# Kernel tuning notes

Hardware: AMD Instinct MI355X
Metric: run time of the kernel (lower is better)

## Reference

```python
import jax, jax.numpy as jnp
import numpy as np

B, T, I = 256, 512, 12   # batch, n_step, input_dims
H, Z = 1024, 128         # hidden_dims, z1_dims


def _gru_step(h, xt, Wih, Whh, bih, bhh):
    # torch GRU/GRUCell gate math; gate order in weights: r, z, n
    gi = xt @ Wih.T + bih            # [B, 3H]
    gh = h @ Whh.T + bhh             # [B, 3H]
    i_r, i_z, i_n = jnp.split(gi, 3, axis=-1)
    h_r, h_z, h_n = jnp.split(gh, 3, axis=-1)
    r = jax.nn.sigmoid(i_r + h_r)
    zg = jax.nn.sigmoid(i_z + h_z)
    n = jnp.tanh(i_n + r * h_n)
    return (1.0 - zg) * n + zg * h


def setup_inputs() -> dict:
    key = jax.random.key(0)
    ks = jax.random.split(key, 24)
    s = 0.03
    d = {
        "x": jax.random.uniform(ks[0], (B, T, I), dtype=jnp.float32),
        "noise": jax.random.normal(ks[1], (B, Z), dtype=jnp.float32),
        # bidirectional GRU encoder (forward / backward directions)
        "W_ih_f": jax.random.normal(ks[2], (3 * H, I)) * s,
        "W_hh_f": jax.random.normal(ks[3], (3 * H, H)) * s,
        "b_ih_f": jnp.zeros((3 * H,), jnp.float32),
        "b_hh_f": jnp.zeros((3 * H,), jnp.float32),
        "W_ih_b": jax.random.normal(ks[4], (3 * H, I)) * s,
        "W_hh_b": jax.random.normal(ks[5], (3 * H, H)) * s,
        "b_ih_b": jnp.zeros((3 * H,), jnp.float32),
        "b_hh_b": jnp.zeros((3 * H,), jnp.float32),
        # mu / var heads over concatenated bidirectional final state [B, 2H]
        "W_mu": jax.random.normal(ks[6], (Z, 2 * H)) * s,
        "b_mu": jnp.zeros((Z,), jnp.float32),
        "W_var": jax.random.normal(ks[7], (Z, 2 * H)) * s,
        "b_var": jnp.zeros((Z,), jnp.float32),
        # decoder
        "W_init": jax.random.normal(ks[8], (H, Z)) * s,
        "b_init": jnp.zeros((H,), jnp.float32),
        "W_out": jax.random.normal(ks[9], (I, H)) * s,
        "b_out": jnp.zeros((I,), jnp.float32),
        "Wc_ih": jax.random.normal(ks[10], (3 * H, I + Z)) * s,
        "Wc_hh": jax.random.normal(ks[11], (3 * H, H)) * s,
        "bc_ih": jnp.zeros((3 * H,), jnp.float32),
        "bc_hh": jnp.zeros((3 * H,), jnp.float32),
    }
    return d


def reference(x, noise, W_ih_f, W_hh_f, b_ih_f, b_hh_f,
              W_ih_b, W_hh_b, b_ih_b, b_hh_b,
              W_mu, b_mu, W_var, b_var,
              W_init, b_init, W_out, b_out,
              Wc_ih, Wc_hh, bc_ih, bc_hh):
    b, t, i = x.shape
    h0 = jnp.zeros((b, W_hh_f.shape[1]), x.dtype)
    xs = jnp.swapaxes(x, 0, 1)  # [T, B, I]

    # ---- encoder: bidirectional GRU, keep only final hidden per direction ----
    def step_f(h, xt):
        return _gru_step(h, xt, W_ih_f, W_hh_f, b_ih_f, b_hh_f), None

    def step_b(h, xt):
        return _gru_step(h, xt, W_ih_b, W_hh_b, b_ih_b, b_hh_b), None

    h_f, _ = jax.lax.scan(step_f, h0, xs)
    h_b, _ = jax.lax.scan(step_b, h0, xs[::-1])
    henc = jnp.concatenate([h_f, h_b], axis=-1)  # [B, 2H] (dir-major, matches torch view)

    mean = henc @ W_mu.T + b_mu
    stddev = jnp.exp(0.5 * (henc @ W_var.T + b_var))
    z = mean + stddev * noise  # rsample (training mode)

    # ---- decoder: GRUCell with teacher forcing (eps starts at 1 -> p < eps) ----
    init_out = jnp.zeros((b, i), x.dtype).at[:, -1].set(1.0)
    teacher = jnp.concatenate([init_out[:, None, :], x[:, :-1, :]], axis=1)  # [B,T,I]
    inps = jnp.swapaxes(teacher, 0, 1)  # [T, B, I]

    hx = jnp.tanh(z @ W_init.T + b_init)

    def dstep(h, inp):
        u = jnp.concatenate([inp, z], axis=1)  # [B, I+Z]
        h = _gru_step(h, u, Wc_ih, Wc_hh, bc_ih, bc_hh)
        out = jax.nn.sigmoid(h @ W_out.T + b_out)
        return h, out

    _, outs = jax.lax.scan(dstep, hx, inps)  # outs: [T, B, I]
    recon = jnp.swapaxes(outs, 0, 1)  # [B, T, I]
    return recon, mean, stddev
```

## Files before the change

kernel.cpp:

```cpp
#include <hip/hip_runtime.h>
#include <cstdint>
#include <cstddef>


typedef _Float16 f16;
typedef _Float16 f16x8 __attribute__((ext_vector_type(8)));
typedef float f32x4 __attribute__((ext_vector_type(4)));

#define NB 256
#define NT 512
#define NI 12
#define NH 1024
#define NZ 128
#define NG 3072
#define KE_ENC 1056
#define KE_DEC 1184
#define XK_ENC 32
#define XK_DEC 160
#define ZXP 40

#define MFMA16(a, b, c) __builtin_amdgcn_mfma_f32_16x16x32_f16((a), (b), (c), 0, 0, 0)

#define OFF_WMF   ((size_t)0)
#define OFF_WMB   (OFF_WMF + (size_t)NG * KE_ENC * 2)
#define OFF_WMD   (OFF_WMB + (size_t)NG * KE_ENC * 2)
#define OFF_WNF   (OFF_WMD + (size_t)NG * KE_DEC * 2)
#define OFF_WNB   (OFF_WNF + (size_t)NH * XK_ENC * 2)
#define OFF_WND   (OFF_WNB + (size_t)NH * XK_ENC * 2)
#define OFF_WOUT  (OFF_WND + (size_t)NH * XK_DEC * 2)
#define OFF_HENC16 (OFF_WOUT + (size_t)16 * KE_ENC * 2)
#define OFF_HF32   (OFF_HENC16 + (size_t)4 * NB * NH * 2)
#define OFF_CTL    (OFF_HF32 + (size_t)2 * NB * NH * 4)
#define OFF_H32D   (OFF_CTL + (size_t)2 * NB * NH * 2)
#define OFF_Z32    (OFF_H32D + (size_t)NB * NH * 4)
#define OFF_Z16    (OFF_Z32 + (size_t)NB * NZ * 4)
#define OFF_FLG    (OFF_Z16 + (size_t)NB * NZ * 2)
#define N_FLG 204800
#define N_FLGD 131072
#define WS_NEEDED (OFF_FLG + (size_t)N_FLG * 4)

#define OUT_MEAN (NB * NT * NI)
#define OUT_STD  (OUT_MEAN + NB * NZ)

__device__ __forceinline__ void wave_spin(const unsigned* base, unsigned tgt,
                                          int lane, int nslots) {
    const unsigned* p = base + (lane & (nslots - 1));
    for (;;) {
        unsigned v = __hip_atomic_load(p, __ATOMIC_RELAXED, __HIP_MEMORY_SCOPE_AGENT);
        if (__all((int)(v == tgt))) break;
        __builtin_amdgcn_s_sleep(1);
    }
}

#define PW(N) do { \
    asm volatile("s_waitcnt vmcnt(%0)" :: "n"(N) : "memory"); \
    __builtin_amdgcn_sched_barrier(0x387); \
} while (0)

__global__ __launch_bounds__(256) void prep_kernel(
    const float* __restrict__ Whhf, const float* __restrict__ Wihf,
    const float* __restrict__ bihf, const float* __restrict__ bhhf,
    const float* __restrict__ Whhb, const float* __restrict__ Wihb,
    const float* __restrict__ bihb, const float* __restrict__ bhhb,
    const float* __restrict__ Wchh, const float* __restrict__ Wcih,
    const float* __restrict__ bcih, const float* __restrict__ bchh,
    const float* __restrict__ Wo,   const float* __restrict__ bo,
    f16* __restrict__ wmf, f16* __restrict__ wmb, f16* __restrict__ wmd,
    f16* __restrict__ wnf, f16* __restrict__ wnb, f16* __restrict__ wnd,
    f16* __restrict__ wout,
    f16* __restrict__ h16e0f, f16* __restrict__ h16e0b,
    unsigned* __restrict__ flgs, unsigned* __restrict__ flgd)
{
    const int gsz = gridDim.x * blockDim.x;
    const int gid = blockIdx.x * blockDim.x + threadIdx.x;

    for (int idx = gid; idx < NG * KE_ENC; idx += gsz) {
        const int c = idx / KE_ENC, k = idx - c * KE_ENC;
        float vf, vb;
        if (k < NH) { vf = Whhf[c * NH + k]; vb = Whhb[c * NH + k]; }
        else {
            const int e = k - NH;
            if (c < 2 * NH) {
                if (e < 12)       { vf = Wihf[c * 12 + e]; vb = Wihb[c * 12 + e]; }
                else if (e == 12) { vf = bihf[c] + bhhf[c]; vb = bihb[c] + bhhb[c]; }
                else              { vf = 0.f; vb = 0.f; }
            } else {
                vf = (e == 12) ? bhhf[c] : 0.f;
                vb = (e == 12) ? bhhb[c] : 0.f;
            }
        }
        wmf[idx] = (f16)vf; wmb[idx] = (f16)vb;
    }
    for (int idx = gid; idx < NG * KE_DEC; idx += gsz) {
        const int c = idx / KE_DEC, k = idx - c * KE_DEC;
        float v;
        if (k < NH) v = Wchh[c * NH + k];
        else {
            const int e = k - NH;
            if (c < 2 * NH) {
                if (e < 12)       v = Wcih[c * 140 + e];
                else if (e == 12) v = bcih[c] + bchh[c];
                else if (e < 32)  v = 0.f;
                else              v = Wcih[c * 140 + 12 + (e - 32)];
            } else v = (e == 12) ? bchh[c] : 0.f;
        }
        wmd[idx] = (f16)v;
    }
    for (int idx = gid; idx < NH * XK_ENC; idx += gsz) {
        const int j = idx >> 5, e = idx & 31;
        const int c = 2 * NH + j;
        float vf, vb;
        if (e < 12)       { vf = Wihf[c * 12 + e]; vb = Wihb[c * 12 + e]; }
        else if (e == 12) { vf = bihf[c]; vb = bihb[c]; }
        else              { vf = 0.f; vb = 0.f; }
        wnf[idx] = (f16)vf; wnb[idx] = (f16)vb;
    }
    for (int idx = gid; idx < NH * XK_DEC; idx += gsz) {
        const int j = idx / XK_DEC, e = idx - j * XK_DEC;
        const int c = 2 * NH + j;
        float v;
        if (e < 12)       v = Wcih[c * 140 + e];
        else if (e == 12) v = bcih[c];
        else if (e < 32)  v = 0.f;
        else              v = Wcih[c * 140 + 12 + (e - 32)];
        wnd[idx] = (f16)v;
    }
    for (int idx = gid; idx < 16 * KE_ENC; idx += gsz) {
        const int i = idx / KE_ENC, k = idx - i * KE_ENC;
        float v = 0.f;
        if (i < 12) {
            if (k < NH) v = Wo[i * NH + k];
            else if (k == NH + 12) v = bo[i];
        }
        wout[idx] = (f16)v;
    }
    for (int idx = gid; idx < NB * NH; idx += gsz) {
        h16e0f[idx] = (f16)0.f; h16e0b[idx] = (f16)0.f;
    }
    for (int idx = gid; idx < N_FLG; idx += gsz) flgs[idx] = 0u;
    for (int idx = gid; idx < N_FLGD; idx += gsz) flgd[idx] = 0u;
}

__global__ __launch_bounds__(256, 1) void enc_kernel(
    const float* __restrict__ x,
    const f16* __restrict__ wmF, const f16* __restrict__ wmB_,
    const f16* __restrict__ wnF, const f16* __restrict__ wnB_,
    f16* __restrict__ hbuf,
    float* __restrict__ hf32,
    unsigned* __restrict__ flg)
{
    constexpr int KE  = KE_ENC;
    constexpr int KEP = KE + 8;

    __shared__ f16 Wlds[48 * KEP];
    __shared__ f16 wext[48 * 36];
    __shared__ f16 wnlds[32 * ZXP];
    __shared__ f16 Zx[64 * ZXP];

    const int tid = threadIdx.x;
    const int bid = blockIdx.x;
    const int w = tid >> 6, lane = tid & 63;
    const int lr = lane & 15, quad = lane >> 4;

    const int chain = bid >> 5;
    const int slice = bid & 31;
    const int dir = chain >> 2;
    const int m0 = (chain & 3) * 64;
    const int j0 = slice * 32;
    const int RB = m0 + (w << 4);

    const f16* wm = dir ? wmB_ : wmF;
    const f16* wn = dir ? wnB_ : wnF;
    f16* hb0 = hbuf + (size_t)dir * 2 * NB * NH;

    constexpr int KQ = KE / 8;
    for (int u = tid; u < 48 * KQ; u += 256) {
        const int r = u / KQ, kk = u - r * KQ;
        const int c = (r >> 4) * NH + j0 + (r & 15);
        *(uint4*)&Wlds[r * KEP + kk * 8] = *(const uint4*)(wm + (size_t)c * KE + kk * 8);
    }
    for (int u = tid; u < 48 * 4; u += 256) {
        const int r = u >> 2, kk = u & 3;
        const int c = (r >> 4) * NH + j0 + 16 + (r & 15);
        *(uint4*)&wext[r * 36 + kk * 8] = *(const uint4*)(wm + (size_t)c * KE + 1024 + kk * 8);
    }
    for (int u = tid; u < 32 * 4; u += 256) {
        const int r = u >> 2, kk = u & 3;
        *(uint4*)&wnlds[r * ZXP + kk * 8] = *(const uint4*)(wn + (size_t)(j0 + r) * XK_ENC + kk * 8);
    }
    for (int u = tid; u < 64 * ZXP / 8; u += 256)
        *(uint4*)&Zx[u * 8] = make_uint4(0u, 0u, 0u, 0u);
    __syncthreads();

    float hmast[2][4];
#pragma unroll
    for (int cs = 0; cs < 2; ++cs)
#pragma unroll
        for (int r = 0; r < 4; ++r) hmast[cs][r] = 0.f;

    unsigned* myflg = flg + (size_t)chain * 512 * 32;

    const char* bg0 = (const char*)wm + 2 * ((size_t)(0 * NH + j0 + 16 + lr) * KE + (quad << 3));
    const char* bg1 = (const char*)wm + 2 * ((size_t)(1 * NH + j0 + 16 + lr) * KE + (quad << 3));
    const char* bg2 = (const char*)wm + 2 * ((size_t)(2 * NH + j0 + 16 + lr) * KE + (quad << 3));

#define EA(c) do { \
    asm volatile( \
        "global_load_dwordx4 %0, %2, off offset:%3 sc0 sc1\n\t" \
        "global_load_dwordx4 %1, %2, off offset:%4 sc0 sc1" \
        : "=&v"(av[(c) & 7][0]), "=&v"(av[(c) & 7][1]) \
        : "v"(ga0), "n"((c) * 128), "n"((c) * 128 + 64) \
        : "memory"); \
} while (0)
#define EB(c) do { \
    asm volatile( \
        "global_load_dwordx4 %0, %6, off offset:%9\n\t" \
        "global_load_dwordx4 %1, %6, off offset:%10\n\t" \
        "global_load_dwordx4 %2, %7, off offset:%9\n\t" \
        "global_load_dwordx4 %3, %7, off offset:%10\n\t" \
        "global_load_dwordx4 %4, %8, off offset:%9\n\t" \
        "global_load_dwordx4 %5, %8, off offset:%10" \
        : "=&v"(bv[(c) & 3][0]), "=&v"(bv[(c) & 3][1]), \
          "=&v"(bv[(c) & 3][2]), "=&v"(bv[(c) & 3][3]), \
          "=&v"(bv[(c) & 3][4]), "=&v"(bv[(c) & 3][5]) \
        : "v"(bg0), "v"(bg1), "v"(bg2), "n"((c) * 128), "n"((c) * 128 + 64) \
        : "memory"); \
} while (0)
#define ECONS(c) do { \
    _Pragma("unroll") \
    for (int kt2_ = 0; kt2_ < 2; ++kt2_) { \
        const int ktg_ = (c) * 2 + kt2_; \
        const f16x8 a_ = av[(c) & 7][kt2_]; \
        _Pragma("unroll") \
        for (int g_ = 0; g_ < 3; ++g_) { \
            const f16x8 bl_ = *(const f16x8*)(&Wlds[(g_ * 16 + lr) * KEP + ktg_ * 32 + (quad << 3)]); \
            acc0[g_] = MFMA16(a_, bl_, acc0[g_]); \
            acc1[g_] = MFMA16(a_, bv[(c) & 3][g_ * 2 + kt2_], acc1[g_]); \
        } \
    } \
} while (0)

#pragma unroll 1
    for (int t = 0; t < NT; ++t) {
        if (tid < 64) {
            f16 rowv[16];
            const int b_ = m0 + tid;
            const int tx = dir ? (NT - 1 - t) : t;
            const float4* xr = (const float4*)(x + ((size_t)b_ * NT + tx) * NI);
            const float4 x0 = xr[0], x1 = xr[1], x2 = xr[2];
            rowv[0] = (f16)x0.x; rowv[1] = (f16)x0.y; rowv[2] = (f16)x0.z; rowv[3] = (f16)x0.w;
            rowv[4] = (f16)x1.x; rowv[5] = (f16)x1.y; rowv[6] = (f16)x1.z; rowv[7] = (f16)x1.w;
            rowv[8] = (f16)x2.x; rowv[9] = (f16)x2.y; rowv[10] = (f16)x2.z; rowv[11] = (f16)x2.w;
            rowv[12] = (f16)1.f; rowv[13] = (f16)0.f; rowv[14] = (f16)0.f; rowv[15] = (f16)0.f;
            *(uint4*)&Zx[tid * ZXP]     = *(const uint4*)&rowv[0];
            *(uint4*)&Zx[tid * ZXP + 8] = *(const uint4*)&rowv[8];
        }
        if (t > 0 && tid < 64)
            wave_spin(myflg + (size_t)(t - 1) * 32, (unsigned)t, lane, 32);
        __syncthreads();

        const f16* hcur = hb0 + (size_t)(t & 1) * (NB * NH);
        const char* ga0 = (const char*)(hcur + (size_t)(RB + lr) * NH) + (quad << 4);

        f32x4 acc0[3], acc1[3];
#pragma unroll
        for (int g = 0; g < 3; ++g) {
            f32x4 zv = {0.f, 0.f, 0.f, 0.f};
            acc0[g] = zv; acc1[g] = zv;
        }
        f32x4 accn0 = {0.f, 0.f, 0.f, 0.f}, accn1 = {0.f, 0.f, 0.f, 0.f};

        f16x8 av[8][2];
        f16x8 bv[4][6];
        EA(0); EA(1); EA(2); EA(3); EA(4);
        EB(0); EB(1); EB(2);
        PW(12); EA(5);  EB(3);  ECONS(0);
        PW(14); EA(6);  EB(4);  ECONS(1);
        PW(16); EA(7);  EB(5);  ECONS(2);
        PW(16); EA(8);  EB(6);  ECONS(3);
        PW(16); EA(9);  EB(7);  ECONS(4);
        PW(16); EA(10); EB(8);  ECONS(5);
        PW(16); EA(11); EB(9);  ECONS(6);
        PW(16); EA(12); EB(10); ECONS(7);
        PW(16); EA(13); EB(11); ECONS(8);
        PW(16); EA(14); EB(12); ECONS(9);
        PW(16); EA(15); EB(13); ECONS(10);
        PW(16); EB(14); ECONS(11);
        PW(14); EB(15); ECONS(12);
        PW(12); ECONS(13);
        PW(6);  ECONS(14);
        PW(0);  ECONS(15);

        {
            const f16x8 a0 = *(const f16x8*)(&Zx[((w << 4) + lr) * ZXP + (quad << 3)]);
#pragma unroll
            for (int g = 0; g < 3; ++g) {
                const f16x8 bl = *(const f16x8*)(&Wlds[(g * 16 + lr) * KEP + 1024 + (quad << 3)]);
                acc0[g] = MFMA16(a0, bl, acc0[g]);
                const f16x8 bs = *(const f16x8*)(&wext[(g * 16 + lr) * 36 + (quad << 3)]);
                acc1[g] = MFMA16(a0, bs, acc1[g]);
            }
            const f16x8 bn0 = *(const f16x8*)(&wnlds[lr * ZXP + (quad << 3)]);
            accn0 = MFMA16(a0, bn0, accn0);
            const f16x8 bn1 = *(const f16x8*)(&wnlds[(16 + lr) * ZXP + (quad << 3)]);
            accn1 = MFMA16(a0, bn1, accn1);
        }

        f16* hnext = hb0 + (size_t)((t + 1) & 1) * (NB * NH);
#pragma unroll
        for (int cs = 0; cs < 2; ++cs) {
#pragma unroll
            for (int r = 0; r < 4; ++r) {
                const float rr  = cs ? acc1[0][r] : acc0[0][r];
                const float zz  = cs ? acc1[1][r] : acc0[1][r];
                const float ghn = cs ? acc1[2][r] : acc0[2][r];
                const float gin = cs ? accn1[r]   : accn0[r];
                const float rg = 1.f / (1.f + __expf(-rr));
                const float zg = 1.f / (1.f + __expf(-zz));
                const float nv = gin + rg * ghn;
                const float e2 = __expf(2.f * nv);
                const float th = 1.f - 2.f / (e2 + 1.f);
                const float hn = (1.f - zg) * th + zg * hmast[cs][r];
                hmast[cs][r] = hn;
                const unsigned hv =
                    (unsigned)__builtin_bit_cast(unsigned short, (f16)hn);
                const unsigned ov = (unsigned)__shfl_xor((int)hv, 1, 64);
                if (!(lr & 1)) {
                    const int row = RB + quad * 4 + r;
                    __hip_atomic_store(
                        (unsigned*)&hnext[(size_t)row * NH + j0 + cs * 16 + lr],
                        hv | (ov << 16),
                        __ATOMIC_RELAXED, __HIP_MEMORY_SCOPE_AGENT);
                }
            }
        }
        __syncthreads();
        if (tid == 0)
            __hip_atomic_store(myflg + (size_t)t * 32 + slice, (unsigned)(t + 1),
                               __ATOMIC_RELAXED, __HIP_MEMORY_SCOPE_AGENT);
    }
#undef EA
#undef EB
#undef ECONS

    {
        float* hdst = hf32 + (size_t)dir * NB * NH;
#pragma unroll
        for (int cs = 0; cs < 2; ++cs)
#pragma unroll
            for (int r = 0; r < 4; ++r) {
                const int row = RB + quad * 4 + r;
                hdst[(size_t)row * NH + j0 + cs * 16 + lr] = hmast[cs][r];
            }
    }
}

template<int MODE>
__global__ __launch_bounds__(256, 1) void persist_kernel(
    const float* __restrict__ x,
    const f16* __restrict__ wmF, const f16* __restrict__ wmB_,
    const f16* __restrict__ wnF, const f16* __restrict__ wnB_,
    const f16* __restrict__ wout, const f16* __restrict__ z16,
    f16* __restrict__ hbuf,
    float* __restrict__ hf32,
    const float* __restrict__ h32i,
    float* __restrict__ dout,
    unsigned* __restrict__ flg)
{
    constexpr int KE  = MODE ? KE_DEC : KE_ENC;
    constexpr int KEP = KE + 8;
    constexpr int XK  = MODE ? XK_DEC : XK_ENC;
    constexpr int XKP = XK + 8;
    constexpr int NZT = MODE ? 4 : 0;
    constexpr int NRT = MODE ? 1 : 2;
    constexpr int MROWS = MODE ? 64 : 128;

    __shared__ f16 Wlds[48 * KEP];
    __shared__ f16 Zx[MROWS * ZXP];
    __shared__ f16 wnlds[16 * XKP];
    __shared__ f16 wolds[MODE ? 16 * 1064 : 8];

    const int tid = threadIdx.x;
    const int bid = blockIdx.x;
    const int w = tid >> 6, lane = tid & 63;
    const int lr = lane & 15, quad = lane >> 4;

    const int chain = bid >> 6;
    const int slice = bid & 63;
    const int dir = MODE ? 0 : (chain >> 1);
    const int m0 = MODE ? chain * 64 : (chain & 1) * 128;
    const int j0 = slice * 16;
    const bool outw = (MODE == 1) && (slice == 0);
    const int RB = m0 + (MODE ? (w << 4) : (w << 5));

    const f16* wm = (MODE == 0 && dir) ? wmB_ : wmF;
    const f16* wn = (MODE == 0 && dir) ? wnB_ : wnF;
    f16* hb0 = hbuf + (MODE ? (size_t)0 : (size_t)dir * 2 * NB * NH);
    constexpr int BMSK = MODE ? 3 : 1;

    constexpr int KQ = KE / 8;
    for (int u = tid; u < 48 * KQ; u += 256) {
        const int r = u / KQ, kk = u - r * KQ;
        const int c = (r >> 4) * NH + j0 + (r & 15);
        *(uint4*)&Wlds[r * KEP + kk * 8] = *(const uint4*)(wm + (size_t)c * KE + kk * 8);
    }
    constexpr int XQ = XK / 8;
    for (int u = tid; u < 16 * XQ; u += 256) {
        const int r = u / XQ, kk = u - r * XQ;
        *(uint4*)&wnlds[r * XKP + kk * 8] =
            *(const uint4*)(wn + (size_t)(j0 + r) * XK + kk * 8);
    }
    if (outw) {
        for (int u = tid; u < 16 * 132; u += 256) {
            const int r = u / 132, kk = u - r * 132;
            *(uint4*)&wolds[r * 1064 + kk * 8] =
                *(const uint4*)(wout + (size_t)r * KE_ENC + kk * 8);
        }
    }
    for (int u = tid; u < MROWS * ZXP / 8; u += 256)
        *(uint4*)&Zx[u * 8] = make_uint4(0u, 0u, 0u, 0u);
    __syncthreads();

    float hmast[2][4];
    f16x8 azr[2][NZT ? NZT : 1];
#pragma unroll
    for (int rt = 0; rt < NRT; ++rt)
#pragma unroll
        for (int r = 0; r < 4; ++r)
            hmast[rt][r] = MODE
                ? h32i[(size_t)(RB + rt * 16 + quad * 4 + r) * NH + j0 + lr]
                : 0.f;
    if (MODE) {
#pragma unroll
        for (int rt = 0; rt < NRT; ++rt)
#pragma unroll
            for (int zt = 0; zt < NZT; ++zt)
                azr[rt][zt] = *(const f16x8*)(z16 +
                    (size_t)(RB + rt * 16 + lr) * NZ + zt * 32 + (quad << 3));
    }
    f16x8 ax;
#pragma unroll
    for (int j = 0; j < 8; ++j) ax[j] = (f16)0.f;
    if (quad == 1) ax[4] = (f16)1.f;

    unsigned* myflg = flg + (size_t)chain * 512 * 64;

#define AISSUE_E(c) do { \
    asm volatile( \
        "global_load_dwordx4 %0, %4, off offset:%6 sc0 sc1\n\t" \
        "global_load_dwordx4 %1, %5, off offset:%6 sc0 sc1\n\t" \
        "global_load_dwordx4 %2, %4, off offset:%7 sc0 sc1\n\t" \
        "global_load_dwordx4 %3, %5, off offset:%7 sc0 sc1" \
        : "=&v"(av[(c) & 15][0]), "=&v"(av[(c) & 15][1]), \
          "=&v"(av[(c) & 15][2]), "=&v"(av[(c) & 15][3]) \
        : "v"(ga0), "v"(ga1), "n"((c) * 128), "n"((c) * 128 + 64) \
        : "memory"); \
} while (0)
#define PCONS_E(c) do { \
    _Pragma("unroll") \
    for (int kt2_ = 0; kt2_ < 2; ++kt2_) { \
        const f16x8 a0_ = av[(c) & 15][kt2_ * 2]; \
        const f16x8 a1_ = av[(c) & 15][kt2_ * 2 + 1]; \
        _Pragma("unroll") \
        for (int g_ = 0; g_ < 3; ++g_) { \
            const f16x8 b_ = *(const f16x8*)(&Wlds[(g_ * 16 + lr) * KEP + ((c) * 2 + kt2_) * 32 + (quad << 3)]); \
            acc[g_][0] = MFMA16(a0_, b_, acc[g_][0]); \
            acc[g_][1] = MFMA16(a1_, b_, acc[g_][1]); \
        } \
    } \
} while (0)
#define AISSUE_D(c) do { \
    asm volatile( \
        "global_load_dwordx4 %0, %2, off offset:%3 sc0 sc1\n\t" \
        "global_load_dwordx4 %1, %2, off offset:%4 sc0 sc1" \
        : "=&v"(av[(c)][0]), "=&v"(av[(c)][1]) \
        : "v"(ga0), "n"((c) * 128), "n"((c) * 128 + 64) \
        : "memory"); \
} while (0)
#define PCONS_D(c) do { \
    _Pragma("unroll") \
    for (int kt2_ = 0; kt2_ < 2; ++kt2_) { \
        const f16x8 a0_ = av[(c)][kt2_]; \
        _Pragma("unroll") \
        for (int g_ = 0; g_ < 3; ++g_) { \
            const f16x8 b_ = *(const f16x8*)(&Wlds[(g_ * 16 + lr) * KEP + ((c) * 2 + kt2_) * 32 + (quad << 3)]); \
            acc[g_][0] = MFMA16(a0_, b_, acc[g_][0]); \
        } \
        if (outw) { \
            const f16x8 bo_ = *(const f16x8*)(&wolds[lr * 1064 + ((c) * 2 + kt2_) * 32 + (quad << 3)]); \
            accq = MFMA16(a0_, bo_, accq); \
        } \
    } \
} while (0)
#define OCONSQ(c) do { \
    _Pragma("unroll") \
    for (int kt2_ = 0; kt2_ < 2; ++kt2_) { \
        const f16x8 bo_ = *(const f16x8*)(&wolds[lr * 1064 + ((c) * 2 + kt2_) * 32 + (quad << 3)]); \
        accq = MFMA16(av[(c)][kt2_], bo_, accq); \
    } \
} while (0)

#pragma unroll 1
    for (int t = 0; t < NT; ++t) {
        if (tid < MROWS) {
            f16 rowv[16];
            if (MODE == 1 && t == 0) {
#pragma unroll
                for (int e = 0; e < 12; ++e) rowv[e] = (f16)((e == NI - 1) ? 1.f : 0.f);
            } else {
                const int b_ = m0 + tid;
                const int tx = MODE ? (t - 1) : (dir ? (NT - 1 - t) : t);
                const float4* xr = (const float4*)(x + ((size_t)b_ * NT + tx) * NI);
                const float4 x0 = xr[0], x1 = xr[1], x2 = xr[2];
                rowv[0] = (f16)x0.x; rowv[1] = (f16)x0.y; rowv[2] = (f16)x0.z; rowv[3] = (f16)x0.w;
                rowv[4] = (f16)x1.x; rowv[5] = (f16)x1.y; rowv[6] = (f16)x1.z; rowv[7] = (f16)x1.w;
                rowv[8] = (f16)x2.x; rowv[9] = (f16)x2.y; rowv[10] = (f16)x2.z; rowv[11] = (f16)x2.w;
            }
            rowv[12] = (f16)1.f; rowv[13] = (f16)0.f; rowv[14] = (f16)0.f; rowv[15] = (f16)0.f;
            *(uint4*)&Zx[tid * ZXP]     = *(const uint4*)&rowv[0];
            *(uint4*)&Zx[tid * ZXP + 8] = *(const uint4*)&rowv[8];
        }
        if (t > 0 && tid < 64)
            wave_spin(myflg + (size_t)(t - 1) * 64, (unsigned)t, lane, 64);
        __syncthreads();

        const f16* hcur = hb0 + (size_t)(t & BMSK) * (NB * NH);
        const char* ga0 = (const char*)(hcur +
            (size_t)(RB + lr) * NH) + (quad << 4);
        const char* ga1 = ga0 + (size_t)16 * NH * 2;
        (void)ga1;

        f32x4 acc[3][2], accn[2];
#pragma unroll
        for (int g = 0; g < 3; ++g)
#pragma unroll
            for (int rt = 0; rt < 2; ++rt) { f32x4 zv = {0.f,0.f,0.f,0.f}; acc[g][rt] = zv; }
        { f32x4 zv = {0.f,0.f,0.f,0.f}; accn[0] = zv; accn[1] = zv; }
        f32x4 accq = {0.f, 0.f, 0.f, 0.f};

        if (MODE == 0) {
            f16x8 av[16][4];
            AISSUE_E(0);  AISSUE_E(1);  AISSUE_E(2);  AISSUE_E(3);
            AISSUE_E(4);  AISSUE_E(5);  AISSUE_E(6);  AISSUE_E(7);
            AISSUE_E(8);  AISSUE_E(9);
            PW(36); PCONS_E(0);  AISSUE_E(10);
            PW(36); PCONS_E(1);  AISSUE_E(11);
            PW(36); PCONS_E(2);  AISSUE_E(12);
            PW(36); PCONS_E(3);  AISSUE_E(13);
            PW(36); PCONS_E(4);  AISSUE_E(14);
            PW(36); PCONS_E(5);  AISSUE_E(15);
            PW(36); PCONS_E(6);
            PW(32); PCONS_E(7);
            PW(28); PCONS_E(8);
            PW(24); PCONS_E(9);
            PW(20); PCONS_E(10);
            PW(16); PCONS_E(11);
            PW(12); PCONS_E(12);
            PW(8);  PCONS_E(13);
            PW(4);  PCONS_E(14);
            PW(0);  PCONS_E(15);
        } else {
            f16x8 av[16][2];
            AISSUE_D(0);  AISSUE_D(1);  AISSUE_D(2);  AISSUE_D(3);
            AISSUE_D(4);  AISSUE_D(5);  AISSUE_D(6);  AISSUE_D(7);
            AISSUE_D(8);  AISSUE_D(9);  AISSUE_D(10); AISSUE_D(11);
            AISSUE_D(12); AISSUE_D(13); AISSUE_D(14); AISSUE_D(15);
            PW(30); PCONS_D(0);
            PW(28); PCONS_D(1);
            PW(26); PCONS_D(2);
            PW(24); PCONS_D(3);
            PW(22); PCONS_D(4);
            PW(20); PCONS_D(5);
            PW(18); PCONS_D(6);
            PW(16); PCONS_D(7);
            PW(14); PCONS_D(8);
            PW(12); PCONS_D(9);
            PW(10); PCONS_D(10);
            PW(8);  PCONS_D(11);
            PW(6);  PCONS_D(12);
            PW(4);  PCONS_D(13);
            PW(2);  PCONS_D(14);
            PW(0);  PCONS_D(15);
        }

#pragma unroll
        for (int xt = 0; xt <= NZT; ++xt) {
            const int kt = 32 + xt;
            f16x8 a0, a1;
            if (xt == 0) {
                a0 = *(const f16x8*)(&Zx[((MODE ? (w << 4) : (w << 5)) + lr) * ZXP + (quad << 3)]);
                if (MODE == 0)
                    a1 = *(const f16x8*)(&Zx[((w << 5) + 16 + lr) * ZXP + (quad << 3)]);
            } else { a0 = azr[0][xt - 1]; if (NRT > 1) a1 = azr[1][xt - 1]; }
#pragma unroll
            for (int g = 0; g < 3; ++g) {
                f16x8 b = *(const f16x8*)(&Wlds[(g * 16 + lr) * KEP + kt * 32 + (quad << 3)]);
                acc[g][0] = MFMA16(a0, b, acc[g][0]);
                if (NRT > 1) acc[g][1] = MFMA16(a1, b, acc[g][1]);
            }
            f16x8 bn = *(const f16x8*)(&wnlds[lr * XKP + xt * 32 + (quad << 3)]);
            accn[0] = MFMA16(a0, bn, accn[0]);
            if (NRT > 1) accn[1] = MFMA16(a1, bn, accn[1]);
        }

        if (outw) {
            const f16x8 bo_ = *(const f16x8*)(&wolds[lr * 1064 + 1024 + (quad << 3)]);
            accq = MFMA16(ax, bo_, accq);
            if (t >= 1 && lr < NI) {
#pragma unroll
                for (int r = 0; r < 4; ++r) {
                    const int b_ = RB + quad * 4 + r;
                    dout[(size_t)b_ * (NT * NI) + (t - 1) * NI + lr] =
                        1.f / (1.f + __expf(-accq[r]));
                }
            }
        }

        f16* hnext = hb0 + (size_t)((t + 1) & BMSK) * (NB * NH);
#pragma unroll
        for (int rt = 0; rt < NRT; ++rt) {
#pragma unroll
            for (int r = 0; r < 4; ++r) {
                const float rr  = acc[0][rt][r];
                const float zz  = acc[1][rt][r];
                const float ghn = acc[2][rt][r];
                const float gin = accn[rt][r];
                const float rg = 1.f / (1.f + __expf(-rr));
                const float zg = 1.f / (1.f + __expf(-zz));
                const float nv = gin + rg * ghn;
                const float e2 = __expf(2.f * nv);
                const float th = 1.f - 2.f / (e2 + 1.f);
                const float hn = (1.f - zg) * th + zg * hmast[rt][r];
                hmast[rt][r] = hn;
                const unsigned hv =
                    (unsigned)__builtin_bit_cast(unsigned short, (f16)hn);
                const unsigned ov = (unsigned)__shfl_xor((int)hv, 1, 64);
                if (!(lr & 1)) {
                    const int row = RB + rt * 16 + quad * 4 + r;
                    __hip_atomic_store(
                        (unsigned*)&hnext[(size_t)row * NH + j0 + lr],
                        hv | (ov << 16),
                        __ATOMIC_RELAXED, __HIP_MEMORY_SCOPE_AGENT);
                }
            }
        }
        __syncthreads();
        if (tid == 0)
            __hip_atomic_store(myflg + (size_t)t * 64 + slice, (unsigned)(t + 1),
                               __ATOMIC_RELAXED, __HIP_MEMORY_SCOPE_AGENT);
    }

    if (MODE == 0) {
        float* hdst = hf32 + (size_t)dir * NB * NH;
#pragma unroll
        for (int rt = 0; rt < NRT; ++rt)
#pragma unroll
            for (int r = 0; r < 4; ++r) {
                const int row = RB + rt * 16 + quad * 4 + r;
                hdst[(size_t)row * NH + j0 + lr] = hmast[rt][r];
            }
    }

    if (MODE == 1 && outw) {
        if (tid < 64)
            wave_spin(myflg + (size_t)511 * 64, 512u, lane, 64);
        __syncthreads();
        const f16* hc = hb0 + (size_t)(512 & BMSK) * (NB * NH);
        const char* ga0 = (const char*)(hc + (size_t)(RB + lr) * NH) + (quad << 4);
        f32x4 accq = {0.f, 0.f, 0.f, 0.f};
        f16x8 av[16][2];
        AISSUE_D(0);  AISSUE_D(1);  AISSUE_D(2);  AISSUE_D(3);
        AISSUE_D(4);  AISSUE_D(5);  AISSUE_D(6);  AISSUE_D(7);
        AISSUE_D(8);  AISSUE_D(9);  AISSUE_D(10); AISSUE_D(11);
        AISSUE_D(12); AISSUE_D(13); AISSUE_D(14); AISSUE_D(15);
        PW(30); OCONSQ(0);
        PW(28); OCONSQ(1);
        PW(26); OCONSQ(2);
        PW(24); OCONSQ(3);
        PW(22); OCONSQ(4);
        PW(20); OCONSQ(5);
        PW(18); OCONSQ(6);
        PW(16); OCONSQ(7);
        PW(14); OCONSQ(8);
        PW(12); OCONSQ(9);
        PW(10); OCONSQ(10);
        PW(8);  OCONSQ(11);
        PW(6);  OCONSQ(12);
        PW(4);  OCONSQ(13);
        PW(2);  OCONSQ(14);
        PW(0);  OCONSQ(15);
        {
            const f16x8 bo_ = *(const f16x8*)(&wolds[lr * 1064 + 1024 + (quad << 3)]);
            accq = MFMA16(ax, bo_, accq);
        }
        if (lr < NI) {
#pragma unroll
            for (int r = 0; r < 4; ++r) {
                const int b_ = RB + quad * 4 + r;
                dout[(size_t)b_ * (NT * NI) + 511 * NI + lr] =
                    1.f / (1.f + __expf(-accq[r]));
            }
        }
    }
#undef AISSUE_E
#undef PCONS_E
#undef AISSUE_D
#undef PCONS_D
#undef OCONSQ
}

__global__ __launch_bounds__(256) void heads1_kernel(
    const float* __restrict__ hf, const float* __restrict__ hb,
    const float* __restrict__ Wmu, const float* __restrict__ bmu,
    const float* __restrict__ Wvar, const float* __restrict__ bvar,
    const float* __restrict__ noise,
    float* __restrict__ dout, float* __restrict__ z32, f16* __restrict__ z16)
{
    const int tid = threadIdx.x;
    const int b  = ((int)blockIdx.x >> 3) * 16 + (tid >> 4);
    const int zi = ((int)blockIdx.x & 7) * 16 + (tid & 15);
    const float4* h4 = (const float4*)(hf + (size_t)b * NH);
    const float4* g4 = (const float4*)(hb + (size_t)b * NH);
    const float4* m4 = (const float4*)(Wmu + (size_t)zi * (2 * NH));
    const float4* v4 = (const float4*)(Wvar + (size_t)zi * (2 * NH));
    float sm_ = 0.f, sv = 0.f;
    for (int k = 0; k < NH / 4; ++k) {
        const float4 h = h4[k], a = m4[k], c = v4[k];
        sm_ += h.x * a.x + h.y * a.y + h.z * a.z + h.w * a.w;
        sv  += h.x * c.x + h.y * c.y + h.z * c.z + h.w * c.w;
    }
    for (int k = 0; k < NH / 4; ++k) {
        const float4 h = g4[k], a = m4[NH / 4 + k], c = v4[NH / 4 + k];
        sm_ += h.x * a.x + h.y * a.y + h.z * a.z + h.w * a.w;
        sv  += h.x * c.x + h.y * c.y + h.z * c.z + h.w * c.w;
    }
    const float mean = sm_ + bmu[zi];
    const float lv   = sv + bvar[zi];
    const float sd   = __expf(0.5f * lv);
    const float zv   = mean + sd * noise[(size_t)b * NZ + zi];
    dout[OUT_MEAN + (size_t)b * NZ + zi] = mean;
    dout[OUT_STD  + (size_t)b * NZ + zi] = sd;
    z32[b * NZ + zi] = zv;
    z16[b * NZ + zi] = (f16)zv;
}

__global__ __launch_bounds__(256) void heads2_kernel(
    const float* __restrict__ z32, const float* __restrict__ Winit,
    const float* __restrict__ binit,
    float* __restrict__ h32d, f16* __restrict__ h16d)
{
    __shared__ float Wi[16 * NZ];
    __shared__ float bi[16];
    const int tid = threadIdx.x;
    const int jb = blockIdx.x;
    for (int f = tid; f < 16 * NZ; f += 256)
        Wi[f] = Winit[(size_t)(jb * 16 + (f >> 7)) * NZ + (f & 127)];
    if (tid < 16) bi[tid] = binit[jb * 16 + tid];
    __syncthreads();
    const int b = tid;
    const float4* z4 = (const float4*)(z32 + (size_t)b * NZ);
    float4 zr[NZ / 4];
#pragma unroll
    for (int k = 0; k < NZ / 4; ++k) zr[k] = z4[k];
    for (int hj = 0; hj < 16; ++hj) {
        const float4* w4 = (const float4*)(Wi + hj * NZ);
        float s = bi[hj];
#pragma unroll
        for (int k = 0; k < NZ / 4; ++k) {
            const float4 a = w4[k], z = zr[k];
            s += z.x * a.x + z.y * a.y + z.z * a.z + z.w * a.w;
        }
        const float e2 = __expf(2.f * s);
        const float th = 1.f - 2.f / (e2 + 1.f);
        h32d[(size_t)b * NH + jb * 16 + hj] = th;
        h16d[(size_t)b * NH + jb * 16 + hj] = (f16)th;
    }
}

extern "C" void kernel_launch(void* const* d_in, const int* in_sizes, int n_in,
                              void* d_out, int out_size, void* d_ws, size_t ws_size,
                              hipStream_t stream)
{
    const float* x     = (const float*)d_in[0];
    const float* noise = (const float*)d_in[1];
    const float* Wihf  = (const float*)d_in[2];
    const float* Whhf  = (const float*)d_in[3];
    const float* bihf  = (const float*)d_in[4];
    const float* bhhf  = (const float*)d_in[5];
    const float* Wihb  = (const float*)d_in[6];
    const float* Whhb  = (const float*)d_in[7];
    const float* bihb  = (const float*)d_in[8];
    const float* bhhb  = (const float*)d_in[9];
    const float* Wmu   = (const float*)d_in[10];
    const float* bmu   = (const float*)d_in[11];
    const float* Wvar  = (const float*)d_in[12];
    const float* bvar  = (const float*)d_in[13];
    const float* Winit = (const float*)d_in[14];
    const float* binit = (const float*)d_in[15];
    const float* Wo    = (const float*)d_in[16];
    const float* bo    = (const float*)d_in[17];
    const float* Wcih  = (const float*)d_in[18];
    const float* Wchh  = (const float*)d_in[19];
    const float* bcih  = (const float*)d_in[20];
    const float* bchh  = (const float*)d_in[21];
    float* dout = (float*)d_out;
    char*  ws   = (char*)d_ws;

    if (ws_size < WS_NEEDED) return;

    f16* wmf  = (f16*)(ws + OFF_WMF);
    f16* wmb  = (f16*)(ws + OFF_WMB);
    f16* wmd  = (f16*)(ws + OFF_WMD);
    f16* wnf  = (f16*)(ws + OFF_WNF);
    f16* wnb  = (f16*)(ws + OFF_WNB);
    f16* wnd  = (f16*)(ws + OFF_WND);
    f16* wo16 = (f16*)(ws + OFF_WOUT);
    f16* h16  = (f16*)(ws + OFF_HENC16);
    float* hf32  = (float*)(ws + OFF_HF32);
    float* h32d  = (float*)(ws + OFF_H32D);
    float* z32p  = (float*)(ws + OFF_Z32);
    f16*   z16p  = (f16*)(ws + OFF_Z16);
    unsigned* flg_e = (unsigned*)(ws + OFF_FLG);
    unsigned* flg_d = (unsigned*)(ws + OFF_CTL);

    prep_kernel<<<2048, 256, 0, stream>>>(
        Whhf, Wihf, bihf, bhhf, Whhb, Wihb, bihb, bhhb,
        Wchh, Wcih, bcih, bchh, Wo, bo,
        wmf, wmb, wmd, wnf, wnb, wnd, wo16,
        h16 , h16 + (size_t)2 * NB * NH ,
        flg_e, flg_d);

    enc_kernel<<<256, 256, 0, stream>>>(
        x, wmf, wmb, wnf, wnb, h16, hf32, flg_e);

    heads1_kernel<<<128, 256, 0, stream>>>(hf32, hf32 + (size_t)NB * NH,
                                           Wmu, bmu, Wvar, bvar, noise,
                                           dout, z32p, z16p);
    heads2_kernel<<<64, 256, 0, stream>>>(z32p, Winit, binit, h32d, h16 );

    persist_kernel<1><<<256, 256, 0, stream>>>(
        x, wmd, (const f16*)nullptr, wnd, (const f16*)nullptr, wo16, z16p,
        h16, (float*)nullptr, h32d, dout, flg_d);
}
```

Measured before the change: 9.902 ms.

## Pre-swizzle encoder weights into per-slice MFMA-fragment layout for contiguous loads

The prep kernel now writes encoder weights in a per-direction, per-slice blocked layout. The streamed B-operand part uses lane-contiguous MFMA fragment order, so each wave's global loads in the recurrent loop are fully coalesced 1KB chunks instead of strided row reads. The extra-column weights are now held in registers instead of a separate LDS array. The unused MODE 0 encoder path of the persistent kernel is also removed. This adds prep work and more index arithmetic during weight reorganisation, and uses a few more registers.

```diff
diff --git a/kernel.cpp b/kernel.cpp
--- a/kernel.cpp
+++ b/kernel.cpp
@@ -19,11 +19,14 @@
 #define XK_DEC 160
 #define ZXP 40
 
+#define WBT_PS 50688
+#define WBT_EXT 49152
+
 #define MFMA16(a, b, c) __builtin_amdgcn_mfma_f32_16x16x32_f16((a), (b), (c), 0, 0, 0)
 
-#define OFF_WMF   ((size_t)0)
-#define OFF_WMB   (OFF_WMF + (size_t)NG * KE_ENC * 2)
-#define OFF_WMD   (OFF_WMB + (size_t)NG * KE_ENC * 2)
+#define OFF_WENC  ((size_t)0)
+#define OFF_WBT   (OFF_WENC + (size_t)2 * 32 * 48 * 1056 * 2)
+#define OFF_WMD   (OFF_WBT + (size_t)2 * 32 * WBT_PS * 2)
 #define OFF_WNF   (OFF_WMD + (size_t)NG * KE_DEC * 2)
 #define OFF_WNB   (OFF_WNF + (size_t)NH * XK_ENC * 2)
 #define OFF_WND   (OFF_WNB + (size_t)NH * XK_ENC * 2)
@@ -57,6 +60,19 @@
     __builtin_amdgcn_sched_barrier(0x387); \
 } while (0)
 
+__device__ __forceinline__ float enc_wval(int c, int k,
+    const float* __restrict__ Whh, const float* __restrict__ Wih,
+    const float* __restrict__ bih, const float* __restrict__ bhh) {
+    if (k < NH) return Whh[(size_t)c * NH + k];
+    const int e = k - NH;
+    if (c < 2 * NH) {
+        if (e < 12)  return Wih[c * 12 + e];
+        if (e == 12) return bih[c] + bhh[c];
+        return 0.f;
+    }
+    return (e == 12) ? bhh[c] : 0.f;
+}
+
 __global__ __launch_bounds__(256) void prep_kernel(
     const float* __restrict__ Whhf, const float* __restrict__ Wihf,
     const float* __restrict__ bihf, const float* __restrict__ bhhf,
@@ -65,7 +81,7 @@
     const float* __restrict__ Wchh, const float* __restrict__ Wcih,
     const float* __restrict__ bcih, const float* __restrict__ bchh,
     const float* __restrict__ Wo,   const float* __restrict__ bo,
-    f16* __restrict__ wmf, f16* __restrict__ wmb, f16* __restrict__ wmd,
+    f16* __restrict__ wenc, f16* __restrict__ wbt, f16* __restrict__ wmd,
     f16* __restrict__ wnf, f16* __restrict__ wnb, f16* __restrict__ wnd,
     f16* __restrict__ wout,
     f16* __restrict__ h16e0f, f16* __restrict__ h16e0b,
@@ -74,22 +90,41 @@
     const int gsz = gridDim.x * blockDim.x;
     const int gid = blockIdx.x * blockDim.x + threadIdx.x;
 
-    for (int idx = gid; idx < NG * KE_ENC; idx += gsz) {
-        const int c = idx / KE_ENC, k = idx - c * KE_ENC;
-        float vf, vb;
-        if (k < NH) { vf = Whhf[c * NH + k]; vb = Whhb[c * NH + k]; }
-        else {
-            const int e = k - NH;
-            if (c < 2 * NH) {
-                if (e < 12)       { vf = Wihf[c * 12 + e]; vb = Wihb[c * 12 + e]; }
-                else if (e == 12) { vf = bihf[c] + bhhf[c]; vb = bihb[c] + bhhb[c]; }
-                else              { vf = 0.f; vb = 0.f; }
-            } else {
-                vf = (e == 12) ? bhhf[c] : 0.f;
-                vb = (e == 12) ? bhhb[c] : 0.f;
-            }
-        }
-        wmf[idx] = (f16)vf; wmb[idx] = (f16)vb;
+    for (int idx = gid; idx < 2 * 32 * 48 * 1056; idx += gsz) {
+        const int d = idx / (32 * 48 * 1056);
+        int rem = idx - d * (32 * 48 * 1056);
+        const int s = rem / (48 * 1056);
+        rem -= s * (48 * 1056);
+        const int r = rem / 1056, k = rem - r * 1056;
+        const int c = (r >> 4) * NH + s * 32 + (r & 15);
+        const float v = d
+            ? enc_wval(c, k, Whhb, Wihb, bihb, bhhb)
+            : enc_wval(c, k, Whhf, Wihf, bihf, bhhf);
+        wenc[idx] = (f16)v;
+    }
+    for (int idx = gid; idx < 2 * 32 * WBT_PS; idx += gsz) {
+        const int d = idx / (32 * WBT_PS);
+        int rem = idx - d * (32 * WBT_PS);
+        const int s = rem / WBT_PS;
+        int q = rem - s * WBT_PS;
+        int g, l, e, k;
+        if (q < WBT_EXT) {
+            const int c = q / 3072; q -= c * 3072;
+            g = q >> 10; q &= 1023;
+            const int kt2 = q >> 9; q &= 511;
+            l = q >> 3; e = q & 7;
+            k = (c * 2 + kt2) * 32 + (l >> 4) * 8 + e;
+        } else {
+            q -= WBT_EXT;
+            g = q >> 9; q &= 511;
+            l = q >> 3; e = q & 7;
+            k = 1024 + (l >> 4) * 8 + e;
+        }
+        const int c_ = g * NH + s * 32 + 16 + (l & 15);
+        const float v = d
+            ? enc_wval(c_, k, Whhb, Wihb, bihb, bhhb)
+            : enc_wval(c_, k, Whhf, Wihf, bihf, bhhf);
+        wbt[idx] = (f16)v;
     }
     for (int idx = gid; idx < NG * KE_DEC; idx += gsz) {
         const int c = idx / KE_DEC, k = idx - c * KE_DEC;
@@ -143,7 +178,7 @@
 
 __global__ __launch_bounds__(256, 1) void enc_kernel(
     const float* __restrict__ x,
-    const f16* __restrict__ wmF, const f16* __restrict__ wmB_,
+    const f16* __restrict__ wenc, const f16* __restrict__ wbt,
     const f16* __restrict__ wnF, const f16* __restrict__ wnB_,
     f16* __restrict__ hbuf,
     float* __restrict__ hf32,
@@ -153,7 +188,6 @@
     constexpr int KEP = KE + 8;
 
     __shared__ f16 Wlds[48 * KEP];
-    __shared__ f16 wext[48 * 36];
     __shared__ f16 wnlds[32 * ZXP];
     __shared__ f16 Zx[64 * ZXP];
 
@@ -169,29 +203,30 @@
     const int j0 = slice * 32;
     const int RB = m0 + (w << 4);
 
-    const f16* wm = dir ? wmB_ : wmF;
     const f16* wn = dir ? wnB_ : wnF;
     f16* hb0 = hbuf + (size_t)dir * 2 * NB * NH;
+    const f16* wenc_s = wenc + (size_t)(dir * 32 + slice) * 48 * 1056;
+    const f16* wbt_s  = wbt  + (size_t)(dir * 32 + slice) * WBT_PS;
 
     constexpr int KQ = KE / 8;
     for (int u = tid; u < 48 * KQ; u += 256) {
         const int r = u / KQ, kk = u - r * KQ;
-        const int c = (r >> 4) * NH + j0 + (r & 15);
-        *(uint4*)&Wlds[r * KEP + kk * 8] = *(const uint4*)(wm + (size_t)c * KE + kk * 8);
-    }
-    for (int u = tid; u < 48 * 4; u += 256) {
-        const int r = u >> 2, kk = u & 3;
-        const int c = (r >> 4) * NH + j0 + 16 + (r & 15);
-        *(uint4*)&wext[r * 36 + kk * 8] = *(const uint4*)(wm + (size_t)c * KE + 1024 + kk * 8);
+        *(uint4*)&Wlds[r * KEP + kk * 8] =
+            *(const uint4*)(wenc_s + (size_t)r * 1056 + kk * 8);
     }
     for (int u = tid; u < 32 * 4; u += 256) {
         const int r = u >> 2, kk = u & 3;
-        *(uint4*)&wnlds[r * ZXP + kk * 8] = *(const uint4*)(wn + (size_t)(j0 + r) * XK_ENC + kk * 8);
+        *(uint4*)&wnlds[r * ZXP + kk * 8] =
+            *(const uint4*)(wn + (size_t)(j0 + r) * XK_ENC + kk * 8);
     }
     for (int u = tid; u < 64 * ZXP / 8; u += 256)
         *(uint4*)&Zx[u * 8] = make_uint4(0u, 0u, 0u, 0u);
     __syncthreads();
 
+    f16x8 bext0 = *(const f16x8*)(wbt_s + WBT_EXT + 0 * 512 + lane * 8);
+    f16x8 bext1 = *(const f16x8*)(wbt_s + WBT_EXT + 1 * 512 + lane * 8);
+    f16x8 bext2 = *(const f16x8*)(wbt_s + WBT_EXT + 2 * 512 + lane * 8);
+
     float hmast[2][4];
 #pragma unroll
     for (int cs = 0; cs < 2; ++cs)
@@ -200,9 +235,7 @@
 
     unsigned* myflg = flg + (size_t)chain * 512 * 32;
 
-    const char* bg0 = (const char*)wm + 2 * ((size_t)(0 * NH + j0 + 16 + lr) * KE + (quad << 3));
-    const char* bg1 = (const char*)wm + 2 * ((size_t)(1 * NH + j0 + 16 + lr) * KE + (quad << 3));
-    const char* bg2 = (const char*)wm + 2 * ((size_t)(2 * NH + j0 + 16 + lr) * KE + (quad << 3));
+    const char* vbB = (const char*)wbt_s + lane * 16;
 
 #define EA(c) do { \
     asm volatile( \
@@ -214,16 +247,16 @@
 } while (0)
 #define EB(c) do { \
     asm volatile( \
-        "global_load_dwordx4 %0, %6, off offset:%9\n\t" \
-        "global_load_dwordx4 %1, %6, off offset:%10\n\t" \
-        "global_load_dwordx4 %2, %7, off offset:%9\n\t" \
-        "global_load_dwordx4 %3, %7, off offset:%10\n\t" \
-        "global_load_dwordx4 %4, %8, off offset:%9\n\t" \
-        "global_load_dwordx4 %5, %8, off offset:%10" \
+        "global_load_dwordx4 %0, %6, off offset:0\n\t" \
+        "global_load_dwordx4 %1, %6, off offset:1024\n\t" \
+        "global_load_dwordx4 %2, %6, off offset:2048\n\t" \
+        "global_load_dwordx4 %3, %6, off offset:3072\n\t" \
+        "global_load_dwordx4 %4, %7, off offset:1024\n\t" \
+        "global_load_dwordx4 %5, %7, off offset:2048" \
         : "=&v"(bv[(c) & 3][0]), "=&v"(bv[(c) & 3][1]), \
           "=&v"(bv[(c) & 3][2]), "=&v"(bv[(c) & 3][3]), \
           "=&v"(bv[(c) & 3][4]), "=&v"(bv[(c) & 3][5]) \
-        : "v"(bg0), "v"(bg1), "v"(bg2), "n"((c) * 128), "n"((c) * 128 + 64) \
+        : "v"(vbB + (size_t)(c) * 6144), "v"(vbB + (size_t)(c) * 6144 + 3072) \
         : "memory"); \
 } while (0)
 #define ECONS(c) do { \
@@ -293,12 +326,20 @@
 
         {
             const f16x8 a0 = *(const f16x8*)(&Zx[((w << 4) + lr) * ZXP + (quad << 3)]);
-#pragma unroll
-            for (int g = 0; g < 3; ++g) {
-                const f16x8 bl = *(const f16x8*)(&Wlds[(g * 16 + lr) * KEP + 1024 + (quad << 3)]);
-                acc0[g] = MFMA16(a0, bl, acc0[g]);
-                const f16x8 bs = *(const f16x8*)(&wext[(g * 16 + lr) * 36 + (quad << 3)]);
-                acc1[g] = MFMA16(a0, bs, acc1[g]);
+            {
+                const f16x8 bl = *(const f16x8*)(&Wlds[(0 * 16 + lr) * KEP + 1024 + (quad << 3)]);
+                acc0[0] = MFMA16(a0, bl, acc0[0]);
+                acc1[0] = MFMA16(a0, bext0, acc1[0]);
+            }
+            {
+                const f16x8 bl = *(const f16x8*)(&Wlds[(1 * 16 + lr) * KEP + 1024 + (quad << 3)]);
+                acc0[1] = MFMA16(a0, bl, acc0[1]);
+                acc1[1] = MFMA16(a0, bext1, acc1[1]);
+            }
+            {
+                const f16x8 bl = *(const f16x8*)(&Wlds[(2 * 16 + lr) * KEP + 1024 + (quad << 3)]);
+                acc0[2] = MFMA16(a0, bl, acc0[2]);
+                acc1[2] = MFMA16(a0, bext2, acc1[2]);
             }
             const f16x8 bn0 = *(const f16x8*)(&wnlds[lr * ZXP + (quad << 3)]);
             accn0 = MFMA16(a0, bn0, accn0);
@@ -445,30 +486,6 @@
 
     unsigned* myflg = flg + (size_t)chain * 512 * 64;
 
-#define AISSUE_E(c) do { \
-    asm volatile( \
-        "global_load_dwordx4 %0, %4, off offset:%6 sc0 sc1\n\t" \
-        "global_load_dwordx4 %1, %5, off offset:%6 sc0 sc1\n\t" \
-        "global_load_dwordx4 %2, %4, off offset:%7 sc0 sc1\n\t" \
-        "global_load_dwordx4 %3, %5, off offset:%7 sc0 sc1" \
-        : "=&v"(av[(c) & 15][0]), "=&v"(av[(c) & 15][1]), \
-          "=&v"(av[(c) & 15][2]), "=&v"(av[(c) & 15][3]) \
-        : "v"(ga0), "v"(ga1), "n"((c) * 128), "n"((c) * 128 + 64) \
-        : "memory"); \
-} while (0)
-#define PCONS_E(c) do { \
-    _Pragma("unroll") \
-    for (int kt2_ = 0; kt2_ < 2; ++kt2_) { \
-        const f16x8 a0_ = av[(c) & 15][kt2_ * 2]; \
-        const f16x8 a1_ = av[(c) & 15][kt2_ * 2 + 1]; \
-        _Pragma("unroll") \
-        for (int g_ = 0; g_ < 3; ++g_) { \
-            const f16x8 b_ = *(const f16x8*)(&Wlds[(g_ * 16 + lr) * KEP + ((c) * 2 + kt2_) * 32 + (quad << 3)]); \
-            acc[g_][0] = MFMA16(a0_, b_, acc[g_][0]); \
-            acc[g_][1] = MFMA16(a1_, b_, acc[g_][1]); \
-        } \
-    } \
-} while (0)
 #define AISSUE_D(c) do { \
     asm volatile( \
         "global_load_dwordx4 %0, %2, off offset:%3 sc0 sc1\n\t" \
@@ -527,8 +544,6 @@
         const f16* hcur = hb0 + (size_t)(t & BMSK) * (NB * NH);
         const char* ga0 = (const char*)(hcur +
             (size_t)(RB + lr) * NH) + (quad << 4);
-        const char* ga1 = ga0 + (size_t)16 * NH * 2;
-        (void)ga1;
 
         f32x4 acc[3][2], accn[2];
 #pragma unroll
@@ -538,28 +553,7 @@
         { f32x4 zv = {0.f,0.f,0.f,0.f}; accn[0] = zv; accn[1] = zv; }
         f32x4 accq = {0.f, 0.f, 0.f, 0.f};
 
-        if (MODE == 0) {
-            f16x8 av[16][4];
-            AISSUE_E(0);  AISSUE_E(1);  AISSUE_E(2);  AISSUE_E(3);
-            AISSUE_E(4);  AISSUE_E(5);  AISSUE_E(6);  AISSUE_E(7);
-            AISSUE_E(8);  AISSUE_E(9);
-            PW(36); PCONS_E(0);  AISSUE_E(10);
-            PW(36); PCONS_E(1);  AISSUE_E(11);
-            PW(36); PCONS_E(2);  AISSUE_E(12);
-            PW(36); PCONS_E(3);  AISSUE_E(13);
-            PW(36); PCONS_E(4);  AISSUE_E(14);
-            PW(36); PCONS_E(5);  AISSUE_E(15);
-            PW(36); PCONS_E(6);
-            PW(32); PCONS_E(7);
-            PW(28); PCONS_E(8);
-            PW(24); PCONS_E(9);
-            PW(20); PCONS_E(10);
-            PW(16); PCONS_E(11);
-            PW(12); PCONS_E(12);
-            PW(8);  PCONS_E(13);
-            PW(4);  PCONS_E(14);
-            PW(0);  PCONS_E(15);
-        } else {
+        {
             f16x8 av[16][2];
             AISSUE_D(0);  AISSUE_D(1);  AISSUE_D(2);  AISSUE_D(3);
             AISSUE_D(4);  AISSUE_D(5);  AISSUE_D(6);  AISSUE_D(7);
@@ -648,17 +642,6 @@
         if (tid == 0)
             __hip_atomic_store(myflg + (size_t)t * 64 + slice, (unsigned)(t + 1),
                                __ATOMIC_RELAXED, __HIP_MEMORY_SCOPE_AGENT);
-    }
-
-    if (MODE == 0) {
-        float* hdst = hf32 + (size_t)dir * NB * NH;
-#pragma unroll
-        for (int rt = 0; rt < NRT; ++rt)
-#pragma unroll
-            for (int r = 0; r < 4; ++r) {
-                const int row = RB + rt * 16 + quad * 4 + r;
-                hdst[(size_t)row * NH + j0 + lr] = hmast[rt][r];
-            }
     }
 
     if (MODE == 1 && outw) {
@@ -702,8 +685,6 @@
             }
         }
     }
-#undef AISSUE_E
-#undef PCONS_E
 #undef AISSUE_D
 #undef PCONS_D
 #undef OCONSQ
@@ -808,14 +789,14 @@
 
     if (ws_size < WS_NEEDED) return;
 
-    f16* wmf  = (f16*)(ws + OFF_WMF);
-    f16* wmb  = (f16*)(ws + OFF_WMB);
-    f16* wmd  = (f16*)(ws + OFF_WMD);
-    f16* wnf  = (f16*)(ws + OFF_WNF);
-    f16* wnb  = (f16*)(ws + OFF_WNB);
-    f16* wnd  = (f16*)(ws + OFF_WND);
-    f16* wo16 = (f16*)(ws + OFF_WOUT);
-    f16* h16  = (f16*)(ws + OFF_HENC16);
+    f16* wencp = (f16*)(ws + OFF_WENC);
+    f16* wbtp  = (f16*)(ws + OFF_WBT);
+    f16* wmd   = (f16*)(ws + OFF_WMD);
+    f16* wnf   = (f16*)(ws + OFF_WNF);
+    f16* wnb   = (f16*)(ws + OFF_WNB);
+    f16* wnd   = (f16*)(ws + OFF_WND);
+    f16* wo16  = (f16*)(ws + OFF_WOUT);
+    f16* h16   = (f16*)(ws + OFF_HENC16);
     float* hf32  = (float*)(ws + OFF_HF32);
     float* h32d  = (float*)(ws + OFF_H32D);
     float* z32p  = (float*)(ws + OFF_Z32);
@@ -826,12 +807,12 @@
     prep_kernel<<<2048, 256, 0, stream>>>(
         Whhf, Wihf, bihf, bhhf, Whhb, Wihb, bihb, bhhb,
         Wchh, Wcih, bcih, bchh, Wo, bo,
-        wmf, wmb, wmd, wnf, wnb, wnd, wo16,
+        wencp, wbtp, wmd, wnf, wnb, wnd, wo16,
         h16 , h16 + (size_t)2 * NB * NH ,
         flg_e, flg_d);
 
     enc_kernel<<<256, 256, 0, stream>>>(
-        x, wmf, wmb, wnf, wnb, h16, hf32, flg_e);
+        x, wencp, wbtp, wnf, wnb, h16, hf32, flg_e);
 
     heads1_kernel<<<128, 256, 0, stream>>>(hf32, hf32 + (size_t)NB * NH,
                                            Wmu, bmu, Wvar, bvar, noise,
```

Measured after the change: 8.651 ms. 1.14x faster.
